# Performance work log

Hardware: AMD Instinct MI355X
Metric: run time of the kernel (lower is better)

The kernel has to match this reference:

```python
import jax, jax.numpy as jnp
import numpy as np
import math

D_MODEL = 1024
NUM_HEADS = 16
D_K = D_MODEL // NUM_HEADS
B, NQ, NK = 2, 2048, 2048


def setup_inputs() -> dict:
    key = jax.random.key(0)
    ks = jax.random.split(key, 14)
    s = 1.0 / math.sqrt(D_MODEL)
    inp = {
        "query": jax.random.normal(ks[0], (B, NQ, D_MODEL), jnp.float32),
        "key": jax.random.normal(ks[1], (B, NK, D_MODEL), jnp.float32),
        "value": jax.random.normal(ks[2], (B, NK, D_MODEL), jnp.float32),
        "mask": jax.random.randint(ks[3], (B, NK), 0, 2, jnp.int32),
        "attn_bias": jax.random.normal(ks[4], (B, NQ, NK), jnp.float32),
        "w_q": jax.random.normal(ks[5], (D_MODEL, D_MODEL), jnp.float32) * s,
        "b_q": jnp.zeros((D_MODEL,), jnp.float32),
        "w_k": jax.random.normal(ks[6], (D_MODEL, D_MODEL), jnp.float32) * s,
        "b_k": jnp.zeros((D_MODEL,), jnp.float32),
        "w_v": jax.random.normal(ks[7], (D_MODEL, D_MODEL), jnp.float32) * s,
        "b_v": jnp.zeros((D_MODEL,), jnp.float32),
        "w_o": jax.random.normal(ks[8], (D_MODEL, D_MODEL), jnp.float32) * s,
        "b_o": jnp.zeros((D_MODEL,), jnp.float32),
    }
    return inp


def reference(query, key, value, mask, attn_bias, w_q, b_q, w_k, b_k, w_v, b_v, w_o, b_o):
    # Linear projections (torch Linear: x @ W^T + b), reshape to [B, H, N, d_k]
    def proj(x, w, b, n):
        return (x @ w.T + b).reshape(x.shape[0], n, NUM_HEADS, D_K).transpose(0, 2, 1, 3)

    Q = proj(query, w_q, b_q, query.shape[1])   # [B,H,Nq,dk]
    K = proj(key, w_k, b_k, key.shape[1])       # [B,H,Nk,dk]
    V = proj(value, w_v, b_v, value.shape[1])   # [B,H,Nk,dk]

    scores = jnp.einsum("bhqd,bhkd->bhqk", Q, K) / math.sqrt(D_K)
    scores = scores + attn_bias[:, None, :, :]           # bias broadcast over heads
    pad = (mask[:, None, None, :] == 0)                   # [B,1,1,Nk]
    scores = jnp.where(pad, jnp.float32(-1e9), scores)
    attn = jax.nn.softmax(scores, axis=-1)                # dropout is identity (eval)
    out = jnp.einsum("bhqk,bhkd->bhqd", attn, V)          # [B,H,Nq,dk]
    out = out.transpose(0, 2, 1, 3).reshape(query.shape[0], query.shape[1], D_MODEL)
    return out @ w_o.T + b_o
```

## Files before the change

### kernel.cpp

```cpp
#include <hip/hip_runtime.h>


typedef short bf16x8 __attribute__((ext_vector_type(8)));
typedef short bf16x4 __attribute__((ext_vector_type(4)));
typedef float f32x4 __attribute__((ext_vector_type(4)));
typedef int i32x4 __attribute__((ext_vector_type(4)));
typedef unsigned short u16;
typedef unsigned short u16x8 __attribute__((ext_vector_type(8)));
typedef unsigned short u16x4 __attribute__((ext_vector_type(4)));

#define MFMA16(a, b, c) __builtin_amdgcn_mfma_f32_16x16x32_bf16((a), (b), (c), 0, 0, 0)
#define GLD16(gp, lp)                                                     \
  __builtin_amdgcn_global_load_lds(                                       \
      (const __attribute__((address_space(1))) void*)(gp),                \
      (__attribute__((address_space(3))) void*)(lp), 16, 0, 0)

#define WAITVM_BAR(N) asm volatile("s_waitcnt vmcnt(" #N ")\ns_barrier" ::: "memory")
#define BAR() asm volatile("s_barrier" ::: "memory")

#if __has_builtin(__builtin_amdgcn_exp2f)
#define EXP2(x) __builtin_amdgcn_exp2f(x)
#else
#define EXP2(x) exp2f(x)
#endif

__device__ __forceinline__ f32x4 MFMA_PV(bf16x4 a, bf16x4 b, f32x4 c) {
#if __has_builtin(__builtin_amdgcn_mfma_f32_16x16x16bf16_1k)
  return __builtin_amdgcn_mfma_f32_16x16x16bf16_1k(a, b, c, 0, 0, 0);
#else
  asm("v_mfma_f32_16x16x16_bf16 %0, %1, %2, %0" : "+v"(c) : "v"(a), "v"(b));
  return c;
#endif
}

__device__ __forceinline__ u16 f2bf(float f) {
  union { float f; unsigned u; } v; v.f = f;
  return (u16)((v.u + 0x7fffu + ((v.u >> 16) & 1u)) >> 16);
}
__device__ __forceinline__ unsigned pk2(float x, float y) {
  union { float f; unsigned u; } a, b;
  a.f = x; b.f = y;
  return ((a.u + 0x8000u) >> 16) | ((b.u + 0x8000u) & 0xffff0000u);
}

struct ConvDesc { const float* src; u16* dst; int n; };
struct ConvArgs { ConvDesc d[7]; };

__device__ __forceinline__ void biasprep_body(const float* __restrict__ bias,
                                              const int* __restrict__ mask,
                                              u16* __restrict__ out, int i) {
  const int o0 = i * 16;
  const int rowg = o0 >> 11;
  const int b = rowg >> 11;
  const int off = o0 & 2047;
  const int a = off >> 6, g = (off >> 4) & 3;
  const float* src = bias + (size_t)rowg * 2048 + a * 64 + g * 4;
  const int* msk = mask + b * 2048 + a * 64 + g * 4;
  u16x8 w0 = {}, w1 = {};
#pragma unroll
  for (int c = 0; c < 4; c++) {
    f32x4 v = *(const f32x4*)(src + c * 16);
    i32x4 m = *(const i32x4*)(msk + c * 16);
#pragma unroll
    for (int j = 0; j < 4; j++) {
      u16 val = (m[j] != 0) ? f2bf(v[j] * 1.44269504f) : (u16)0xFF80;
      if (c < 2) w0[c * 4 + j] = val;
      else       w1[(c - 2) * 4 + j] = val;
    }
  }
  *(u16x8*)(out + o0) = w0;
  *(u16x8*)(out + o0 + 8) = w1;
}

__global__ __launch_bounds__(256)
void k_prep(ConvArgs a, const float* __restrict__ bias,
            const int* __restrict__ mask, u16* __restrict__ bout) {
  if (blockIdx.y == 7) {
    biasprep_body(bias, mask, bout, blockIdx.x * 256 + threadIdx.x);
    return;
  }
  ConvDesc cd = a.d[blockIdx.y];
  int i = (blockIdx.x * 256 + threadIdx.x) * 8;
  if (i >= cd.n) return;
  const float4* s = (const float4*)(cd.src + i);
  float4 f0 = s[0], f1 = s[1];
  u16x8 o;
  o[0] = f2bf(f0.x); o[1] = f2bf(f0.y); o[2] = f2bf(f0.z); o[3] = f2bf(f0.w);
  o[4] = f2bf(f1.x); o[5] = f2bf(f1.y); o[6] = f2bf(f1.z); o[7] = f2bf(f1.w);
  *(u16x8*)(cd.dst + i) = o;
}

__global__ __launch_bounds__(256)
void k_biasprep(const float* __restrict__ bias, const int* __restrict__ mask,
                u16* __restrict__ out) {
  biasprep_body(bias, mask, out, blockIdx.x * 256 + threadIdx.x);
}

template <int MF>
__device__ __forceinline__ void gemm_impl(const u16* __restrict__ A,
                                          const u16* __restrict__ Bw,
                                          const float* __restrict__ bias,
                                          void* __restrict__ outp, int mode,
                                          float oscale) {
  __shared__ u16 As[2][MF * 1024];
  __shared__ u16 Bs[2][4096];
  const int tid = threadIdx.x;
  const int lane = tid & 63;
  const int wv = tid >> 6;
  const int wr = wv >> 1, wc = wv & 1;
  const int m0 = blockIdx.y * (MF * 32), n0 = blockIdx.x * 128;

  f32x4 acc[MF][4] = {};

  const int s0 = tid, s1 = 256 + tid;
  const int r0 = s0 >> 2, c0 = (s0 & 3) ^ (r0 & 3);
  const int r1 = s1 >> 2, c1 = (s1 & 3) ^ (r1 & 3);
  const u16* gA0 = A + (size_t)(m0 + r0) * 1024 + c0 * 8;
  const u16* gA1 = A + (size_t)(m0 + r1) * 1024 + c1 * 8;
  const u16* gB0 = Bw + (size_t)(n0 + r0) * 1024 + c0 * 8;
  const u16* gB1 = Bw + (size_t)(n0 + r1) * 1024 + c1 * 8;
  u16* lA0 = &As[0][(tid & ~63) * 8];
  u16* lB0 = &Bs[0][(tid & ~63) * 8];

  GLD16(gA0, lA0);
  if constexpr (MF == 4) GLD16(gA1, lA0 + 2048);
  GLD16(gB0, lB0);
  GLD16(gB1, lB0 + 2048);
  WAITVM_BAR(0);

#define GSTEP(BUF, K0)                                                     \
  {                                                                        \
    const int nk = ((K0) + 32) & 1023;                                     \
    GLD16(gA0 + nk, lA0 + ((BUF) ^ 1) * (MF * 1024));                      \
    if constexpr (MF == 4)                                                 \
      GLD16(gA1 + nk, lA0 + 2048 + ((BUF) ^ 1) * (MF * 1024));             \
    GLD16(gB0 + nk, lB0 + ((BUF) ^ 1) * 4096);                             \
    GLD16(gB1 + nk, lB0 + 2048 + ((BUF) ^ 1) * 4096);                      \
    if constexpr (MF == 4) { WAITVM_BAR(4); } else { WAITVM_BAR(3); }      \
    bf16x8 af[MF], bfr[4];                                                 \
    _Pragma("unroll")                                                      \
    for (int mi = 0; mi < MF; mi++) {                                      \
      int row = wr * (MF * 16) + mi * 16 + (lane & 15);                    \
      int byt = row * 64 + (((lane >> 4) * 16) ^ ((row & 3) << 4));        \
      af[mi] = *(const bf16x8*)((const char*)&As[BUF][0] + byt);           \
    }                                                                      \
    _Pragma("unroll")                                                      \
    for (int ni = 0; ni < 4; ni++) {                                       \
      int row = wc * 64 + ni * 16 + (lane & 15);                           \
      int byt = row * 64 + (((lane >> 4) * 16) ^ ((row & 3) << 4));        \
      bfr[ni] = *(const bf16x8*)((const char*)&Bs[BUF][0] + byt);          \
    }                                                                      \
    __builtin_amdgcn_s_setprio(1);                                         \
    _Pragma("unroll")                                                      \
    for (int mi = 0; mi < MF; mi++)                                        \
      _Pragma("unroll")                                                    \
      for (int ni = 0; ni < 4; ni++)                                       \
        acc[mi][ni] = MFMA16(af[mi], bfr[ni], acc[mi][ni]);                \
    __builtin_amdgcn_s_setprio(0);                                         \
    BAR();                                                                 \
  }

  for (int k0 = 0; k0 < 1024; k0 += 64) {
    GSTEP(0, k0)
    GSTEP(1, k0 + 32)
  }
#undef GSTEP

#pragma unroll
  for (int ni = 0; ni < 4; ni++) {
    int n = n0 + wc * 64 + ni * 16 + (lane & 15);
    float bv = bias[n];
#pragma unroll
    for (int mi = 0; mi < MF; mi++) {
      int mb = m0 + wr * (MF * 16) + mi * 16 + (lane >> 4) * 4;
      if (mode == 2) {
        float* O = (float*)outp;
#pragma unroll
        for (int r = 0; r < 4; r++)
          O[(size_t)(mb + r) * 1024 + n] = (acc[mi][ni][r] + bv) * oscale;
      } else if (mode == 0) {
        u16* O = (u16*)outp;
        int b = mb >> 11, q = mb & 2047;
        int h = n >> 6, dk = n & 63;
        size_t base = ((size_t)(b * 16 + h) * 2048 + q) * 64 + dk;
#pragma unroll
        for (int r = 0; r < 4; r++)
          O[base + (size_t)r * 64] = f2bf((acc[mi][ni][r] + bv) * oscale);
      } else {
        u16* O = (u16*)outp;
        int b = mb >> 11, kv = mb & 2047;
        int h = n >> 6, dk = n & 63;
        u16x4 pk;
#pragma unroll
        for (int r = 0; r < 4; r++) pk[r] = f2bf((acc[mi][ni][r] + bv) * oscale);
        *(u16x4*)((u16*)O + ((size_t)((b * 16 + h) * 64 + dk)) * 2048 + kv) = pk;
      }
    }
  }
}

struct GemmDesc { const u16* A; const u16* W; const float* bias; void* out;
                  int mode; float oscale; };
struct Gemm3 { GemmDesc d[3]; };

__global__ __launch_bounds__(256, 2) void k_gemm_qkv(Gemm3 g3) {
  GemmDesc gd = g3.d[blockIdx.z];
  gemm_impl<4>(gd.A, gd.W, gd.bias, gd.out, gd.mode, gd.oscale);
}
__global__ __launch_bounds__(256, 2)
void k_gemm_o(const u16* __restrict__ A, const u16* __restrict__ W,
              const float* __restrict__ bias, float* __restrict__ out) {
  gemm_impl<2>(A, W, bias, out, 2, 1.0f);
}

__global__ __launch_bounds__(512, 4)
void k_attn(const u16* __restrict__ Qb, const u16* __restrict__ Kb,
            const u16* __restrict__ Vt, const u16* __restrict__ BiasE,
            u16* __restrict__ Ob) {
  __shared__ u16 Ks[2][64 * 64];
  __shared__ u16 Vs[2][64 * 64];

  const int tid = threadIdx.x, lane = tid & 63, w = tid >> 6;
  const int g = lane >> 4, q = lane & 15;
  const int h = blockIdx.x, b = blockIdx.y, qt = blockIdx.z;
  const int q0 = qt * 128;
  const size_t bh = (size_t)(b * 16 + h);

  const u16* Qrow = Qb + (bh * 2048 + q0 + w * 16 + q) * 64;
  bf16x8 bq0 = *(const bf16x8*)(Qrow + g * 8);
  bf16x8 bq1 = *(const bf16x8*)(Qrow + 32 + g * 8);

  f32x4 acc[4] = {};
  float mrun = -1e30f, lrun = 0.f;

  const int r0 = tid >> 3, c0 = (tid & 7) ^ (r0 & 7);
  const u16* Kg = Kb + bh * 2048 * 64;
  const u16* Vg = Vt + bh * 64 * 2048;
  const int ld0 = (tid & ~63) * 8;

  const u16* brow = BiasE + ((size_t)b * 2048 + q0 + w * 16 + q) * 2048 + g * 16;

  GLD16(Kg + (size_t)r0 * 64 + c0 * 8, &Ks[0][ld0]);
  GLD16(Vg + (size_t)r0 * 2048 + c0 * 8, &Vs[0][ld0]);
  WAITVM_BAR(0);
  u16x8 bbA0 = *(const u16x8*)(brow);
  u16x8 bbA1 = *(const u16x8*)(brow + 8);
  u16x8 bbB0 = {}, bbB1 = {};

#define ATTN_STEP(BUF, B0, B1, NB0, NB1, T)                                   \
  {                                                                           \
    const int nkv = (((T) + 1) & 31) * 64;                                    \
    GLD16(Kg + (size_t)(nkv + r0) * 64 + c0 * 8, &Ks[(BUF) ^ 1][ld0]);        \
    GLD16(Vg + (size_t)r0 * 2048 + nkv + c0 * 8, &Vs[(BUF) ^ 1][ld0]);        \
    NB0 = *(const u16x8*)(brow + nkv);                                        \
    NB1 = *(const u16x8*)(brow + nkv + 8);                                    \
    WAITVM_BAR(4);                                                            \
    f32x4 sc[4];                                                              \
    __builtin_amdgcn_s_setprio(1);                                            \
    _Pragma("unroll")                                                         \
    for (int c = 0; c < 4; c++) {                                             \
      const int kvr = c * 16 + q;                                             \
      f32x4 z = {};                                                           \
      bf16x8 ak0 = *(const bf16x8*)((const char*)&Ks[BUF][0] + kvr * 128 +    \
                                    ((g * 16) ^ ((kvr & 7) << 4)));           \
      bf16x8 ak1 = *(const bf16x8*)((const char*)&Ks[BUF][0] + kvr * 128 +    \
                                    ((64 + g * 16) ^ ((kvr & 7) << 4)));      \
      z = MFMA16(ak0, bq0, z);                                                \
      z = MFMA16(ak1, bq1, z);                                                \
      sc[c] = z;                                                              \
    }                                                                         \
    __builtin_amdgcn_s_setprio(0);                                            \
    float p[4][4];                                                            \
    float tmax = -3e38f;                                                      \
    _Pragma("unroll")                                                         \
    for (int c = 0; c < 4; c++) {                                             \
      _Pragma("unroll")                                                       \
      for (int r = 0; r < 4; r++) {                                           \
        unsigned braw =                                                       \
            (unsigned)(c < 2 ? (B0)[c * 4 + r] : (B1)[(c - 2) * 4 + r]);      \
        float s = sc[c][r] + __uint_as_float(braw << 16);                     \
        p[c][r] = s;                                                          \
        tmax = fmaxf(tmax, s);                                                \
      }                                                                       \
    }                                                                         \
    tmax = fmaxf(tmax, __shfl_xor(tmax, 16, 64));                             \
    tmax = fmaxf(tmax, __shfl_xor(tmax, 32, 64));                             \
    if (__any(tmax > mrun)) {                                                 \
      float mnew = fmaxf(mrun, tmax);                                         \
      float alpha = EXP2(mrun - mnew);                                        \
      mrun = mnew;                                                            \
      lrun *= alpha;                                                          \
      _Pragma("unroll")                                                       \
      for (int j = 0; j < 4; j++) {                                           \
        float aj = __shfl(alpha, g * 4 + j, 64);                              \
        _Pragma("unroll")                                                     \
        for (int d = 0; d < 4; d++) acc[d][j] *= aj;                          \
      }                                                                       \
    }                                                                         \
    float rsum = 0.f;                                                         \
    _Pragma("unroll")                                                         \
    for (int c = 0; c < 4; c++)                                               \
      _Pragma("unroll")                                                       \
      for (int r = 0; r < 4; r++) {                                           \
        p[c][r] = EXP2(p[c][r] - mrun);                                       \
        rsum += p[c][r];                                                      \
      }                                                                       \
    rsum += __shfl_xor(rsum, 16, 64);                                         \
    rsum += __shfl_xor(rsum, 32, 64);                                         \
    lrun += rsum;                                                             \
    __builtin_amdgcn_s_setprio(1);                                            \
    _Pragma("unroll")                                                         \
    for (int c = 0; c < 4; c++) {                                             \
      union { unsigned u[2]; bf16x4 v; } pa;                                  \
      pa.u[0] = pk2(p[c][0], p[c][1]);                                        \
      pa.u[1] = pk2(p[c][2], p[c][3]);                                        \
      _Pragma("unroll")                                                       \
      for (int d = 0; d < 4; d++) {                                           \
        const int dr = d * 16 + q;                                            \
        bf16x4 vb = *(const bf16x4*)((const char*)&Vs[BUF][0] + dr * 128 +    \
                                     ((c * 32 + g * 8) ^ ((dr & 7) << 4)));   \
        acc[d] = MFMA_PV(pa.v, vb, acc[d]);                                   \
      }                                                                       \
    }                                                                         \
    __builtin_amdgcn_s_setprio(0);                                            \
    BAR();                                                                    \
  }

  for (int t = 0; t < 32; t += 2) {
    ATTN_STEP(0, bbA0, bbA1, bbB0, bbB1, t)
    ATTN_STEP(1, bbB0, bbB1, bbA0, bbA1, t + 1)
  }
#undef ATTN_STEP

  float linv = 1.0f / lrun;
#pragma unroll
  for (int j = 0; j < 4; j++) {
    float li = __shfl(linv, g * 4 + j, 64);
    int qq = q0 + w * 16 + g * 4 + j;
#pragma unroll
    for (int d = 0; d < 4; d++)
      Ob[((size_t)b * 2048 + qq) * 1024 + h * 64 + d * 16 + q] =
          f2bf(acc[d][j] * li);
  }
}

extern "C" void kernel_launch(void* const* d_in, const int* in_sizes, int n_in,
                              void* d_out, int out_size, void* d_ws,
                              size_t ws_size, hipStream_t stream) {
  (void)in_sizes; (void)n_in; (void)out_size;
  const float* q_in = (const float*)d_in[0];
  const float* k_in = (const float*)d_in[1];
  const float* v_in = (const float*)d_in[2];
  const int* mask = (const int*)d_in[3];
  const float* attn_bias = (const float*)d_in[4];
  const float* w_q = (const float*)d_in[5];
  const float* b_q = (const float*)d_in[6];
  const float* w_k = (const float*)d_in[7];
  const float* b_k = (const float*)d_in[8];
  const float* w_v = (const float*)d_in[9];
  const float* b_v = (const float*)d_in[10];
  const float* w_o = (const float*)d_in[11];
  const float* b_o = (const float*)d_in[12];

  const size_t MB = 1u << 20;
  char* ws = (char*)d_ws;
  u16* XQ = (u16*)(ws + 0 * MB);
  u16* XK = (u16*)(ws + 8 * MB);
  u16* XV = (u16*)(ws + 16 * MB);
  u16* WQ = (u16*)(ws + 24 * MB);
  u16* WK = (u16*)(ws + 26 * MB);
  u16* WV = (u16*)(ws + 28 * MB);
  u16* WO = (u16*)(ws + 30 * MB);
  u16* Qb = (u16*)(ws + 32 * MB);
  u16* Kb = (u16*)(ws + 40 * MB);
  u16* Vt = (u16*)(ws + 48 * MB);
  u16* Ob = (u16*)(ws + 56 * MB);
  const bool merged = ws_size >= (size_t)80 * MB;
  u16* BiasE = (u16*)(ws + (merged ? 64 : 0) * MB);

  ConvArgs ca;
  ca.d[0] = {q_in, XQ, 4096 * 1024};
  ca.d[1] = {k_in, XK, 4096 * 1024};
  ca.d[2] = {v_in, XV, 4096 * 1024};
  ca.d[3] = {w_q, WQ, 1024 * 1024};
  ca.d[4] = {w_k, WK, 1024 * 1024};
  ca.d[5] = {w_v, WV, 1024 * 1024};
  ca.d[6] = {w_o, WO, 1024 * 1024};
  k_prep<<<dim3(2048, merged ? 8 : 7), 256, 0, stream>>>(ca, attn_bias, mask,
                                                         BiasE);

  const float QSCALE = 0.125f * 1.44269504f;
  Gemm3 g3;
  g3.d[0] = {XQ, WQ, b_q, (void*)Qb, 0, QSCALE};
  g3.d[1] = {XK, WK, b_k, (void*)Kb, 0, 1.0f};
  g3.d[2] = {XV, WV, b_v, (void*)Vt, 1, 1.0f};
  k_gemm_qkv<<<dim3(8, 32, 3), 256, 0, stream>>>(g3);

  if (!merged) k_biasprep<<<2048, 256, 0, stream>>>(attn_bias, mask, BiasE);

  k_attn<<<dim3(16, 2, 16), 512, 0, stream>>>(Qb, Kb, Vt, BiasE, Ob);

  k_gemm_o<<<dim3(8, 64), 256, 0, stream>>>(Ob, WO, b_o, (float*)d_out);
}
```

Measured before the change: 160.9 us.

## Double KV tile to 128, fold bias into MFMA init, remap blocks per XCD

The attention kernel now processes 128 key/value rows per step instead of 64, halving loop iterations and barriers. It also seeds the QK^T MFMA accumulators with the bias so no separate add is needed. Next-tile prefetch now happens after the QK^T MFMAs and before the softmax, with a single wait-plus-barrier at the top of each step. Blocks use a flat grid remapped so that each XCD handles contiguous head/batch pairs, for better L2 locality of K/V. The larger tiles double LDS use per block, which may lower occupancy, and the full vmcnt(0) wait exposes more load latency.

```diff
diff --git a/kernel.cpp b/kernel.cpp
--- a/kernel.cpp
+++ b/kernel.cpp
@@ -217,12 +217,16 @@
 void k_attn(const u16* __restrict__ Qb, const u16* __restrict__ Kb,
             const u16* __restrict__ Vt, const u16* __restrict__ BiasE,
             u16* __restrict__ Ob) {
-  __shared__ u16 Ks[2][64 * 64];
-  __shared__ u16 Vs[2][64 * 64];
+  __shared__ u16 Ks[2][128 * 64];
+  __shared__ u16 Vs[2][64 * 128];
 
   const int tid = threadIdx.x, lane = tid & 63, w = tid >> 6;
   const int g = lane >> 4, q = lane & 15;
-  const int h = blockIdx.x, b = blockIdx.y, qt = blockIdx.z;
+  const int bid = blockIdx.x;
+  const int xcd = bid & 7, rr = bid >> 3;
+  const int qt = rr & 15;
+  const int pr = xcd + 8 * (rr >> 4);
+  const int b = pr >> 4, h = pr & 15;
   const int q0 = qt * 128;
   const size_t bh = (size_t)(b * 16 + h);
 
@@ -233,102 +237,112 @@
   f32x4 acc[4] = {};
   float mrun = -1e30f, lrun = 0.f;
 
-  const int r0 = tid >> 3, c0 = (tid & 7) ^ (r0 & 7);
+  const int sK1 = tid + 512;
+  const int rK0 = tid >> 3, cK0 = (tid & 7) ^ (rK0 & 7);
+  const int rK1 = sK1 >> 3, cK1 = (sK1 & 7) ^ (rK1 & 7);
+  const int rV0 = tid >> 4, cV0 = (tid & 15) ^ (rV0 & 7);
+  const int rV1 = sK1 >> 4, cV1 = (sK1 & 15) ^ (rV1 & 7);
   const u16* Kg = Kb + bh * 2048 * 64;
   const u16* Vg = Vt + bh * 64 * 2048;
-  const int ld0 = (tid & ~63) * 8;
+  const int ld0 = (tid & ~63) * 8, ld1 = ld0 + 4096;
 
   const u16* brow = BiasE + ((size_t)b * 2048 + q0 + w * 16 + q) * 2048 + g * 16;
 
-  GLD16(Kg + (size_t)r0 * 64 + c0 * 8, &Ks[0][ld0]);
-  GLD16(Vg + (size_t)r0 * 2048 + c0 * 8, &Vs[0][ld0]);
-  WAITVM_BAR(0);
-  u16x8 bbA0 = *(const u16x8*)(brow);
-  u16x8 bbA1 = *(const u16x8*)(brow + 8);
-  u16x8 bbB0 = {}, bbB1 = {};
-
-#define ATTN_STEP(BUF, B0, B1, NB0, NB1, T)                                   \
-  {                                                                           \
-    const int nkv = (((T) + 1) & 31) * 64;                                    \
-    GLD16(Kg + (size_t)(nkv + r0) * 64 + c0 * 8, &Ks[(BUF) ^ 1][ld0]);        \
-    GLD16(Vg + (size_t)r0 * 2048 + nkv + c0 * 8, &Vs[(BUF) ^ 1][ld0]);        \
-    NB0 = *(const u16x8*)(brow + nkv);                                        \
-    NB1 = *(const u16x8*)(brow + nkv + 8);                                    \
-    WAITVM_BAR(4);                                                            \
-    f32x4 sc[4];                                                              \
-    __builtin_amdgcn_s_setprio(1);                                            \
-    _Pragma("unroll")                                                         \
-    for (int c = 0; c < 4; c++) {                                             \
-      const int kvr = c * 16 + q;                                             \
-      f32x4 z = {};                                                           \
-      bf16x8 ak0 = *(const bf16x8*)((const char*)&Ks[BUF][0] + kvr * 128 +    \
-                                    ((g * 16) ^ ((kvr & 7) << 4)));           \
-      bf16x8 ak1 = *(const bf16x8*)((const char*)&Ks[BUF][0] + kvr * 128 +    \
-                                    ((64 + g * 16) ^ ((kvr & 7) << 4)));      \
-      z = MFMA16(ak0, bq0, z);                                                \
-      z = MFMA16(ak1, bq1, z);                                                \
-      sc[c] = z;                                                              \
-    }                                                                         \
-    __builtin_amdgcn_s_setprio(0);                                            \
-    float p[4][4];                                                            \
-    float tmax = -3e38f;                                                      \
-    _Pragma("unroll")                                                         \
-    for (int c = 0; c < 4; c++) {                                             \
-      _Pragma("unroll")                                                       \
-      for (int r = 0; r < 4; r++) {                                           \
-        unsigned braw =                                                       \
-            (unsigned)(c < 2 ? (B0)[c * 4 + r] : (B1)[(c - 2) * 4 + r]);      \
-        float s = sc[c][r] + __uint_as_float(braw << 16);                     \
-        p[c][r] = s;                                                          \
-        tmax = fmaxf(tmax, s);                                                \
-      }                                                                       \
-    }                                                                         \
-    tmax = fmaxf(tmax, __shfl_xor(tmax, 16, 64));                             \
-    tmax = fmaxf(tmax, __shfl_xor(tmax, 32, 64));                             \
-    if (__any(tmax > mrun)) {                                                 \
-      float mnew = fmaxf(mrun, tmax);                                         \
-      float alpha = EXP2(mrun - mnew);                                        \
-      mrun = mnew;                                                            \
-      lrun *= alpha;                                                          \
-      _Pragma("unroll")                                                       \
-      for (int j = 0; j < 4; j++) {                                           \
-        float aj = __shfl(alpha, g * 4 + j, 64);                              \
-        _Pragma("unroll")                                                     \
-        for (int d = 0; d < 4; d++) acc[d][j] *= aj;                          \
-      }                                                                       \
-    }                                                                         \
-    float rsum = 0.f;                                                         \
-    _Pragma("unroll")                                                         \
-    for (int c = 0; c < 4; c++)                                               \
-      _Pragma("unroll")                                                       \
-      for (int r = 0; r < 4; r++) {                                           \
-        p[c][r] = EXP2(p[c][r] - mrun);                                       \
-        rsum += p[c][r];                                                      \
-      }                                                                       \
-    rsum += __shfl_xor(rsum, 16, 64);                                         \
-    rsum += __shfl_xor(rsum, 32, 64);                                         \
-    lrun += rsum;                                                             \
-    __builtin_amdgcn_s_setprio(1);                                            \
-    _Pragma("unroll")                                                         \
-    for (int c = 0; c < 4; c++) {                                             \
-      union { unsigned u[2]; bf16x4 v; } pa;                                  \
-      pa.u[0] = pk2(p[c][0], p[c][1]);                                        \
-      pa.u[1] = pk2(p[c][2], p[c][3]);                                        \
-      _Pragma("unroll")                                                       \
-      for (int d = 0; d < 4; d++) {                                           \
-        const int dr = d * 16 + q;                                            \
-        bf16x4 vb = *(const bf16x4*)((const char*)&Vs[BUF][0] + dr * 128 +    \
-                                     ((c * 32 + g * 8) ^ ((dr & 7) << 4)));   \
-        acc[d] = MFMA_PV(pa.v, vb, acc[d]);                                   \
-      }                                                                       \
-    }                                                                         \
-    __builtin_amdgcn_s_setprio(0);                                            \
-    BAR();                                                                    \
-  }
-
-  for (int t = 0; t < 32; t += 2) {
-    ATTN_STEP(0, bbA0, bbA1, bbB0, bbB1, t)
-    ATTN_STEP(1, bbB0, bbB1, bbA0, bbA1, t + 1)
+  GLD16(Kg + (size_t)rK0 * 64 + cK0 * 8, &Ks[0][ld0]);
+  GLD16(Kg + (size_t)rK1 * 64 + cK1 * 8, &Ks[0][ld1]);
+  GLD16(Vg + (size_t)rV0 * 2048 + cV0 * 8, &Vs[0][ld0]);
+  GLD16(Vg + (size_t)rV1 * 2048 + cV1 * 8, &Vs[0][ld1]);
+  u16x8 bb0 = *(const u16x8*)(brow);
+  u16x8 bb1 = *(const u16x8*)(brow + 8);
+  u16x8 bb2 = *(const u16x8*)(brow + 64);
+  u16x8 bb3 = *(const u16x8*)(brow + 72);
+
+#define ATTN_STEP(BUF, T)                                                      \
+  {                                                                            \
+    WAITVM_BAR(0);            \
+    f32x4 sc[8];                                                               \
+    __builtin_amdgcn_s_setprio(1);                                             \
+    _Pragma("unroll")                                                          \
+    for (int c = 0; c < 8; c++) {                                              \
+      const int kvr = c * 16 + q;                                              \
+      bf16x8 ak0 = *(const bf16x8*)((const char*)&Ks[BUF][0] + kvr * 128 +     \
+                                    ((g * 16) ^ ((kvr & 7) << 4)));            \
+      bf16x8 ak1 = *(const bf16x8*)((const char*)&Ks[BUF][0] + kvr * 128 +     \
+                                    ((64 + g * 16) ^ ((kvr & 7) << 4)));       \
+      const u16x8 blo = (c & 4) ? bb2 : bb0;                                   \
+      const u16x8 bhi = (c & 4) ? bb3 : bb1;                                   \
+      f32x4 cin;                                                               \
+      _Pragma("unroll")                                                        \
+      for (int r = 0; r < 4; r++) {                                            \
+        unsigned braw = (unsigned)(((c & 3) < 2)                               \
+                                       ? blo[(c & 3) * 4 + r]                  \
+                                       : bhi[((c & 3) - 2) * 4 + r]);          \
+        cin[r] = __uint_as_float(braw << 16);                                  \
+      }                                                                        \
+      f32x4 z = MFMA16(ak0, bq0, cin);                                         \
+      sc[c] = MFMA16(ak1, bq1, z);                                             \
+    }                                                                          \
+    __builtin_amdgcn_s_setprio(0);                                             \
+    const int nkv = (((T) + 1) & 15) * 128;                                    \
+    GLD16(Kg + (size_t)(nkv + rK0) * 64 + cK0 * 8, &Ks[(BUF) ^ 1][ld0]);       \
+    GLD16(Kg + (size_t)(nkv + rK1) * 64 + cK1 * 8, &Ks[(BUF) ^ 1][ld1]);       \
+    GLD16(Vg + (size_t)rV0 * 2048 + nkv + cV0 * 8, &Vs[(BUF) ^ 1][ld0]);       \
+    GLD16(Vg + (size_t)rV1 * 2048 + nkv + cV1 * 8, &Vs[(BUF) ^ 1][ld1]);       \
+    bb0 = *(const u16x8*)(brow + nkv);                                         \
+    bb1 = *(const u16x8*)(brow + nkv + 8);                                     \
+    bb2 = *(const u16x8*)(brow + nkv + 64);                                    \
+    bb3 = *(const u16x8*)(brow + nkv + 72);                                    \
+    float tmax = -3e38f;                                                       \
+    _Pragma("unroll")                                                          \
+    for (int c = 0; c < 8; c++)                                                \
+      _Pragma("unroll")                                                        \
+      for (int r = 0; r < 4; r++) tmax = fmaxf(tmax, sc[c][r]);                \
+    tmax = fmaxf(tmax, __shfl_xor(tmax, 16, 64));                              \
+    tmax = fmaxf(tmax, __shfl_xor(tmax, 32, 64));                              \
+    if (__any(tmax > mrun)) {                                                  \
+      float mnew = fmaxf(mrun, tmax);                                          \
+      float alpha = EXP2(mrun - mnew);                                         \
+      mrun = mnew;                                                             \
+      lrun *= alpha;                                                           \
+      _Pragma("unroll")                                                        \
+      for (int j = 0; j < 4; j++) {                                            \
+        float aj = __shfl(alpha, g * 4 + j, 64);                               \
+        _Pragma("unroll")                                                      \
+        for (int d = 0; d < 4; d++) acc[d][j] *= aj;                           \
+      }                                                                        \
+    }                                                                          \
+    float rsum = 0.f;                                                          \
+    float pp[8][4];                                                            \
+    _Pragma("unroll")                                                          \
+    for (int c = 0; c < 8; c++)                                                \
+      _Pragma("unroll")                                                        \
+      for (int r = 0; r < 4; r++) {                                            \
+        pp[c][r] = EXP2(sc[c][r] - mrun);                                      \
+        rsum += pp[c][r];                                                      \
+      }                                                                        \
+    rsum += __shfl_xor(rsum, 16, 64);                                          \
+    rsum += __shfl_xor(rsum, 32, 64);                                          \
+    lrun += rsum;                                                              \
+    __builtin_amdgcn_s_setprio(1);                                             \
+    _Pragma("unroll")                                                          \
+    for (int c = 0; c < 8; c++) {                                              \
+      union { unsigned u[2]; bf16x4 v; } pa;                                   \
+      pa.u[0] = pk2(pp[c][0], pp[c][1]);                                       \
+      pa.u[1] = pk2(pp[c][2], pp[c][3]);                                       \
+      _Pragma("unroll")                                                        \
+      for (int d = 0; d < 4; d++) {                                            \
+        const int dr = d * 16 + q;                                             \
+        bf16x4 vb = *(const bf16x4*)((const char*)&Vs[BUF][0] + dr * 256 +     \
+                                     ((c * 32 + g * 8) ^ ((dr & 7) << 4)));    \
+        acc[d] = MFMA_PV(pa.v, vb, acc[d]);                                    \
+      }                                                                        \
+    }                                                                          \
+    __builtin_amdgcn_s_setprio(0);                                             \
+  }
+
+  for (int t = 0; t < 16; t += 2) {
+    ATTN_STEP(0, t)
+    ATTN_STEP(1, t + 1)
   }
 #undef ATTN_STEP
 
@@ -398,7 +412,7 @@
 
   if (!merged) k_biasprep<<<2048, 256, 0, stream>>>(attn_bias, mask, BiasE);
 
-  k_attn<<<dim3(16, 2, 16), 512, 0, stream>>>(Qb, Kb, Vt, BiasE, Ob);
+  k_attn<<<512, 512, 0, stream>>>(Qb, Kb, Vt, BiasE, Ob);
 
   k_gemm_o<<<dim3(8, 64), 256, 0, stream>>>(Ob, WO, b_o, (float*)d_out);
 }
```

Result: faster. 152.1 us (-5.5%).
